# Kernel tuning notes

Measured on AMD Instinct MI355X. Metric: run time of the kernel, lower is better.

The kernel has to match this reference:

```python
import jax, jax.numpy as jnp
import numpy as np

B, N, D, M, C = 4, 256, 128, 128, 128


def _lin_init(key, din, dout):
    # torch nn.Linear default: U(-1/sqrt(din), 1/sqrt(din)) for weight and bias
    bound = 1.0 / np.sqrt(din)
    kw, kb = jax.random.split(key)
    W = jax.random.uniform(kw, (din, dout), jnp.float32, -bound, bound)
    b = jax.random.uniform(kb, (dout,), jnp.float32, -bound, bound)
    return W, b


def setup_inputs() -> dict:
    key = jax.random.key(0)
    k_h, k_adj, k1, k2, k3, k4 = jax.random.split(key, 6)
    h = jax.random.normal(k_h, (B, N, D), jnp.float32)
    adj = jax.random.uniform(k_adj, (B, N, N), jnp.float32)
    # msg MLP: Linear(2D -> M), SiLU, Linear(M -> M). Split first weight into
    # the h_i block (W1a) and h_j block (W1b) of the concatenated input.
    W1, b1 = _lin_init(k1, 2 * D, M)
    W1a, W1b = W1[:D], W1[D:]
    W2, b2 = _lin_init(k2, M, M)
    # to_c MLP: Linear(M -> M), SiLU, Linear(M -> C)
    Wc1, bc1 = _lin_init(k3, M, M)
    Wc2, bc2 = _lin_init(k4, M, C)
    return {"h": h, "adj": adj, "W1a": W1a, "W1b": W1b, "b1": b1,
            "W2": W2, "b2": b2, "Wc1": Wc1, "bc1": bc1, "Wc2": Wc2, "bc2": bc2}


def reference(h, adj, W1a, W1b, b1, W2, b2, Wc1, bc1, Wc2, bc2):
    n = h.shape[1]
    # First msg Linear on cat([h_i, h_j]) == h_i @ W1a + h_j @ W1b + b1.
    # Precompute per-node projections once instead of the (B,N,N,2D) pair tensor.
    pi = jnp.einsum('bnd,dm->bnm', h, W1a)           # (B,N,M) for destination i
    pj = jnp.einsum('bnd,dm->bnm', h, W1b)           # (B,N,M) for source j
    pre = pi[:, :, None, :] + pj[:, None, :, :] + b1  # (B,N,N,M)
    m = jnp.einsum('bijm,mk->bijk', jax.nn.silu(pre), W2) + b2  # (B,N,N,M)
    # zero self-messages (diagonal ignored), then weight by adjacency
    mask = (1.0 - jnp.eye(n, dtype=h.dtype))[None, :, :, None]
    m = m * mask * adj[..., None]
    # mean aggregation over source nodes j with clamped degree
    denom = jnp.clip(jnp.sum(adj, axis=-1, keepdims=True), 1.0)  # (B,N,1)
    m_agg = jnp.sum(m, axis=2) / denom                           # (B,N,M)
    c = jnp.einsum('bnm,mc->bnc', jax.nn.silu(jnp.einsum('bnm,mk->bnk', m_agg, Wc1) + bc1), Wc2) + bc2
    return c
```

## Files before the change

kernel.cpp:

```cpp
#include <hip/hip_runtime.h>
#include <math.h>

#define BB 4
#define NN 256
#define DD 128
#define MM 128
#define CC 128
#define ROWS (BB * NN)

static __device__ __forceinline__ float fast_exp2(float x) {
#if __has_builtin(__builtin_amdgcn_exp2f)
    return __builtin_amdgcn_exp2f(x);
#else
    return __exp2f(x);
#endif
}

static __device__ __forceinline__ float fast_rcp(float x) {
#if __has_builtin(__builtin_amdgcn_rcpf)
    return __builtin_amdgcn_rcpf(x);
#else
    return 1.0f / x;
#endif
}

static __device__ __forceinline__ float silu_f(float x) {
    float e = fast_exp2(-1.44269504088896340736f * x);
    return x * fast_rcp(1.0f + e);
}

template <int R>
__global__ __launch_bounds__(256) void k_proj(const float* __restrict__ h,
                                              const float* __restrict__ W1a,
                                              const float* __restrict__ W1b,
                                              const float* __restrict__ b1,
                                              float* __restrict__ pibias,
                                              float* __restrict__ pj) {
    __shared__ float sH[R * DD];
    __shared__ float sPA[R][MM];
    __shared__ float sPB[R][MM];
    const int t = threadIdx.x;
    const int m = t & 127;
    const int dh = t >> 7;
    const int row0 = blockIdx.x * R;

    const float* hbase = h + (size_t)row0 * DD;
    sH[t] = hbase[t];
    sH[t + 256] = hbase[t + 256];
    __syncthreads();

    const int d0 = dh * 64;
    float accA[R], accB[R];
    #pragma unroll
    for (int r = 0; r < R; ++r) { accA[r] = 0.0f; accB[r] = 0.0f; }

    #pragma unroll 8
    for (int d = d0; d < d0 + 64; ++d) {
        const float wa = W1a[d * MM + m];
        const float wb = W1b[d * MM + m];
        #pragma unroll
        for (int r = 0; r < R; ++r) {
            const float hv = sH[r * DD + d];
            accA[r] = fmaf(hv, wa, accA[r]);
            accB[r] = fmaf(hv, wb, accB[r]);
        }
    }

    if (dh == 1) {
        #pragma unroll
        for (int r = 0; r < R; ++r) { sPA[r][m] = accA[r]; sPB[r][m] = accB[r]; }
    }
    __syncthreads();
    if (dh == 0) {
        const float bias = b1[m];
        #pragma unroll
        for (int r = 0; r < R; ++r) {
            pibias[(row0 + r) * MM + m] = accA[r] + sPA[r][m] + bias;
            pj[(row0 + r) * MM + m]     = accB[r] + sPB[r][m];
        }
    }
}

__global__ __launch_bounds__(256) void k_msg(const float* __restrict__ adj,
                                             const float* __restrict__ pibias,
                                             const float* __restrict__ pj,
                                             float* __restrict__ S,
                                             float* __restrict__ beta) {
    __shared__ float sAdj[2][NN];
    __shared__ float sRed0[256];
    __shared__ float sRed1[256];
    __shared__ float sWred[2][4];

    const int t = threadIdx.x;
    const int pairIdx = blockIdx.x;
    const int b = pairIdx >> 7;
    const int i0 = (pairIdx & 127) * 2;
    const int row0 = b * NN + i0;

    const float* arow = adj + (size_t)row0 * NN;
    sAdj[0][t] = arow[t];
    sAdj[1][t] = arow[t + 256];
    __syncthreads();

    float v0 = sAdj[0][t];
    float v1 = sAdj[1][t];
    #pragma unroll
    for (int off = 32; off > 0; off >>= 1) {
        v0 += __shfl_xor(v0, off, 64);
        v1 += __shfl_xor(v1, off, 64);
    }
    if ((t & 63) == 0) { sWred[0][t >> 6] = v0; sWred[1][t >> 6] = v1; }
    __syncthreads();
    const float A0 = sWred[0][0] + sWred[0][1] + sWred[0][2] + sWred[0][3];
    const float A1 = sWred[1][0] + sWred[1][1] + sWred[1][2] + sWred[1][3];
    const float aii0 = sAdj[0][i0];
    const float aii1 = sAdj[1][i0 + 1];
    __syncthreads();
    if (t == 0) { sAdj[0][i0] = 0.0f; sAdj[1][i0 + 1] = 0.0f; }
    __syncthreads();

    const float inv0 = 1.0f / fmaxf(A0, 1.0f);
    const float inv1 = 1.0f / fmaxf(A1, 1.0f);

    const int m = t & 127;
    const int jh = t >> 7;
    const float pim0 = pibias[(size_t)row0 * MM + m];
    const float pim1 = pibias[(size_t)(row0 + 1) * MM + m];
    const float* __restrict__ pjB = pj + (size_t)b * NN * MM;

    float acc0 = 0.0f, acc1 = 0.0f;
    #pragma unroll 8
    for (int j = jh; j < NN; j += 2) {
        const float pjv = pjB[j * MM + m];
        const float w0 = sAdj[0][j];
        const float w1 = sAdj[1][j];
        acc0 = fmaf(w0, silu_f(pim0 + pjv), acc0);
        acc1 = fmaf(w1, silu_f(pim1 + pjv), acc1);
    }

    sRed0[t] = acc0;
    sRed1[t] = acc1;
    __syncthreads();
    if (t < 128) {
        S[(size_t)row0 * MM + t] = (sRed0[t] + sRed0[t + 128]) * inv0;
    } else {
        const int k = t - 128;
        S[(size_t)(row0 + 1) * MM + k] = (sRed1[k] + sRed1[k + 128]) * inv1;
    }
    if (t == 0) {
        beta[row0]     = (A0 - aii0) * inv0;
        beta[row0 + 1] = (A1 - aii1) * inv1;
    }
}

__device__ __forceinline__ void stage_dot4(const float* __restrict__ W,
                                           const float sCur[4][MM],
                                           int d0, int k, float acc[4]) {
    #pragma unroll
    for (int r = 0; r < 4; ++r) acc[r] = 0.0f;
    #pragma unroll 8
    for (int d = d0; d < d0 + 64; ++d) {
        const float wv = W[d * MM + k];
        #pragma unroll
        for (int r = 0; r < 4; ++r) acc[r] = fmaf(sCur[r][d], wv, acc[r]);
    }
}

template <int R>
__global__ __launch_bounds__(256) void k_out(const float* __restrict__ S,
                                             const float* __restrict__ beta,
                                             const float* __restrict__ W2,
                                             const float* __restrict__ b2,
                                             const float* __restrict__ Wc1,
                                             const float* __restrict__ bc1,
                                             const float* __restrict__ Wc2,
                                             const float* __restrict__ bc2,
                                             float* __restrict__ out) {
    __shared__ float sA[R][MM];
    __shared__ float sB[R][MM];
    __shared__ float sP[R][MM];
    const int t = threadIdx.x;
    const int k = t & 127;
    const int dh = t >> 7;
    const int d0 = dh * 64;
    const int row0 = blockIdx.x * R;

    float bet[R];
    #pragma unroll
    for (int r = 0; r < R; ++r) bet[r] = beta[row0 + r];

    {
        const float* sbase = S + (size_t)row0 * MM;
        ((float*)sA)[t]       = sbase[t];
        ((float*)sA)[t + 256] = sbase[t + 256];
    }
    __syncthreads();

    float acc[R];

    stage_dot4(W2, sA, d0, k, acc);
    if (dh == 1) {
        #pragma unroll
        for (int r = 0; r < R; ++r) sP[r][k] = acc[r];
    }
    __syncthreads();
    if (dh == 0) {
        const float b2k = b2[k];
        #pragma unroll
        for (int r = 0; r < R; ++r) sB[r][k] = acc[r] + sP[r][k] + bet[r] * b2k;
    }
    __syncthreads();

    stage_dot4(Wc1, sB, d0, k, acc);
    if (dh == 1) {
        #pragma unroll
        for (int r = 0; r < R; ++r) sP[r][k] = acc[r];
    }
    __syncthreads();
    if (dh == 0) {
        const float bc1k = bc1[k];
        #pragma unroll
        for (int r = 0; r < R; ++r) sA[r][k] = silu_f(acc[r] + sP[r][k] + bc1k);
    }
    __syncthreads();

    stage_dot4(Wc2, sA, d0, k, acc);
    if (dh == 1) {
        #pragma unroll
        for (int r = 0; r < R; ++r) sP[r][k] = acc[r];
    }
    __syncthreads();
    if (dh == 0) {
        const float bc2k = bc2[k];
        #pragma unroll
        for (int r = 0; r < R; ++r)
            out[(size_t)(row0 + r) * CC + k] = acc[r] + sP[r][k] + bc2k;
    }
}

extern "C" void kernel_launch(void* const* d_in, const int* in_sizes, int n_in,
                              void* d_out, int out_size, void* d_ws, size_t ws_size,
                              hipStream_t stream) {
    const float* h   = (const float*)d_in[0];
    const float* adj = (const float*)d_in[1];
    const float* W1a = (const float*)d_in[2];
    const float* W1b = (const float*)d_in[3];
    const float* b1  = (const float*)d_in[4];
    const float* W2  = (const float*)d_in[5];
    const float* b2  = (const float*)d_in[6];
    const float* Wc1 = (const float*)d_in[7];
    const float* bc1 = (const float*)d_in[8];
    const float* Wc2 = (const float*)d_in[9];
    const float* bc2 = (const float*)d_in[10];
    float* out = (float*)d_out;

    float* ws = (float*)d_ws;
    float* pibias = ws;
    float* pj     = ws + (size_t)ROWS * MM;
    float* S      = ws + (size_t)2 * ROWS * MM;
    float* beta   = ws + (size_t)3 * ROWS * MM;

    k_proj<4><<<ROWS / 4, 256, 0, stream>>>(h, W1a, W1b, b1, pibias, pj);
    k_msg<<<ROWS / 2, 256, 0, stream>>>(adj, pibias, pj, S, beta);
    k_out<4><<<ROWS / 4, 256, 0, stream>>>(S, beta, W2, b2, Wc1, bc1, Wc2, bc2, out);
}
```

Before: 104.8 us.

## Stage weights and pj tiles in LDS with float4 loads; split work by rows

All three kernels now copy weight or pj tiles into shared memory in chunks using float4 global loads, then compute from LDS instead of strided global reads. The projection and output kernels split threads by row pairs rather than by halves of the reduction dimension, which removes the shared-memory partial-sum combine step. The message kernel also hoists the adjacency and pibias loads ahead of the first barrier. The cost is more barriers per chunk and much larger LDS use per block, which may lower occupancy.

```diff
diff --git a/kernel.cpp b/kernel.cpp
--- a/kernel.cpp
+++ b/kernel.cpp
@@ -36,48 +36,56 @@
                                               const float* __restrict__ b1,
                                               float* __restrict__ pibias,
                                               float* __restrict__ pj) {
+    __shared__ float sWa[32 * MM];
+    __shared__ float sWb[32 * MM];
     __shared__ float sH[R * DD];
-    __shared__ float sPA[R][MM];
-    __shared__ float sPB[R][MM];
+
     const int t = threadIdx.x;
     const int m = t & 127;
-    const int dh = t >> 7;
+    const int rh = t >> 7;
     const int row0 = blockIdx.x * R;
+
+    const float bias = b1[m];
 
     const float* hbase = h + (size_t)row0 * DD;
     sH[t] = hbase[t];
     sH[t + 256] = hbase[t + 256];
-    __syncthreads();
-
-    const int d0 = dh * 64;
-    float accA[R], accB[R];
+
+    float accA[2] = {0.0f, 0.0f};
+    float accB[2] = {0.0f, 0.0f};
+
+    for (int c = 0; c < 4; ++c) {
+        __syncthreads();
+        const float4* ga = (const float4*)(W1a + (size_t)c * 32 * MM);
+        const float4* gb = (const float4*)(W1b + (size_t)c * 32 * MM);
+        float4* la = (float4*)sWa;
+        float4* lb = (float4*)sWb;
+        #pragma unroll
+        for (int i = 0; i < 4; ++i) {
+            la[t + 256 * i] = ga[t + 256 * i];
+            lb[t + 256 * i] = gb[t + 256 * i];
+        }
+        __syncthreads();
+
+        #pragma unroll 8
+        for (int dd = 0; dd < 32; ++dd) {
+            const int d = c * 32 + dd;
+            const float wa = sWa[dd * MM + m];
+            const float wb = sWb[dd * MM + m];
+            #pragma unroll
+            for (int r = 0; r < 2; ++r) {
+                const float hv = sH[(rh * 2 + r) * DD + d];
+                accA[r] = fmaf(hv, wa, accA[r]);
+                accB[r] = fmaf(hv, wb, accB[r]);
+            }
+        }
+    }
+
     #pragma unroll
-    for (int r = 0; r < R; ++r) { accA[r] = 0.0f; accB[r] = 0.0f; }
-
-    #pragma unroll 8
-    for (int d = d0; d < d0 + 64; ++d) {
-        const float wa = W1a[d * MM + m];
-        const float wb = W1b[d * MM + m];
-        #pragma unroll
-        for (int r = 0; r < R; ++r) {
-            const float hv = sH[r * DD + d];
-            accA[r] = fmaf(hv, wa, accA[r]);
-            accB[r] = fmaf(hv, wb, accB[r]);
-        }
-    }
-
-    if (dh == 1) {
-        #pragma unroll
-        for (int r = 0; r < R; ++r) { sPA[r][m] = accA[r]; sPB[r][m] = accB[r]; }
-    }
-    __syncthreads();
-    if (dh == 0) {
-        const float bias = b1[m];
-        #pragma unroll
-        for (int r = 0; r < R; ++r) {
-            pibias[(row0 + r) * MM + m] = accA[r] + sPA[r][m] + bias;
-            pj[(row0 + r) * MM + m]     = accB[r] + sPB[r][m];
-        }
+    for (int r = 0; r < 2; ++r) {
+        const int row = row0 + rh * 2 + r;
+        pibias[(size_t)row * MM + m] = accA[r] + bias;
+        pj[(size_t)row * MM + m]     = accB[r];
     }
 }
 
@@ -86,9 +94,9 @@
                                              const float* __restrict__ pj,
                                              float* __restrict__ S,
                                              float* __restrict__ beta) {
+    __shared__ float sPJ[64 * MM];
     __shared__ float sAdj[2][NN];
-    __shared__ float sRed0[256];
-    __shared__ float sRed1[256];
+    __shared__ float sRed[2][256];
     __shared__ float sWred[2][4];
 
     const int t = threadIdx.x;
@@ -97,13 +105,20 @@
     const int i0 = (pairIdx & 127) * 2;
     const int row0 = b * NN + i0;
 
+    const int m = t & 127;
+    const int jh = t >> 7;
+
     const float* arow = adj + (size_t)row0 * NN;
-    sAdj[0][t] = arow[t];
-    sAdj[1][t] = arow[t + 256];
-    __syncthreads();
-
-    float v0 = sAdj[0][t];
-    float v1 = sAdj[1][t];
+    const float a0v = arow[t];
+    const float a1v = arow[t + 256];
+    const float pim0 = pibias[(size_t)row0 * MM + m];
+    const float pim1 = pibias[(size_t)(row0 + 1) * MM + m];
+
+    sAdj[0][t] = a0v;
+    sAdj[1][t] = a1v;
+    __syncthreads();
+
+    float v0 = a0v, v1 = a1v;
     #pragma unroll
     for (int off = 32; off > 0; off >>= 1) {
         v0 += __shfl_xor(v0, off, 64);
@@ -117,35 +132,40 @@
     const float aii1 = sAdj[1][i0 + 1];
     __syncthreads();
     if (t == 0) { sAdj[0][i0] = 0.0f; sAdj[1][i0 + 1] = 0.0f; }
-    __syncthreads();
 
     const float inv0 = 1.0f / fmaxf(A0, 1.0f);
     const float inv1 = 1.0f / fmaxf(A1, 1.0f);
 
-    const int m = t & 127;
-    const int jh = t >> 7;
-    const float pim0 = pibias[(size_t)row0 * MM + m];
-    const float pim1 = pibias[(size_t)(row0 + 1) * MM + m];
     const float* __restrict__ pjB = pj + (size_t)b * NN * MM;
 
     float acc0 = 0.0f, acc1 = 0.0f;
-    #pragma unroll 8
-    for (int j = jh; j < NN; j += 2) {
-        const float pjv = pjB[j * MM + m];
-        const float w0 = sAdj[0][j];
-        const float w1 = sAdj[1][j];
-        acc0 = fmaf(w0, silu_f(pim0 + pjv), acc0);
-        acc1 = fmaf(w1, silu_f(pim1 + pjv), acc1);
-    }
-
-    sRed0[t] = acc0;
-    sRed1[t] = acc1;
+    for (int c = 0; c < 4; ++c) {
+        __syncthreads();
+        const float4* g = (const float4*)(pjB + (size_t)c * 64 * MM);
+        float4* l = (float4*)sPJ;
+        #pragma unroll
+        for (int i = 0; i < 8; ++i) l[t + 256 * i] = g[t + 256 * i];
+        __syncthreads();
+
+        #pragma unroll 8
+        for (int jj = jh; jj < 64; jj += 2) {
+            const int j = c * 64 + jj;
+            const float pjv = sPJ[jj * MM + m];
+            const float w0 = sAdj[0][j];
+            const float w1 = sAdj[1][j];
+            acc0 = fmaf(w0, silu_f(pim0 + pjv), acc0);
+            acc1 = fmaf(w1, silu_f(pim1 + pjv), acc1);
+        }
+    }
+
+    sRed[0][t] = acc0;
+    sRed[1][t] = acc1;
     __syncthreads();
     if (t < 128) {
-        S[(size_t)row0 * MM + t] = (sRed0[t] + sRed0[t + 128]) * inv0;
+        S[(size_t)row0 * MM + t] = (sRed[0][t] + sRed[0][t + 128]) * inv0;
     } else {
         const int k = t - 128;
-        S[(size_t)(row0 + 1) * MM + k] = (sRed1[k] + sRed1[k + 128]) * inv1;
+        S[(size_t)(row0 + 1) * MM + k] = (sRed[1][k] + sRed[1][k + 128]) * inv1;
     }
     if (t == 0) {
         beta[row0]     = (A0 - aii0) * inv0;
@@ -153,16 +173,25 @@
     }
 }
 
-__device__ __forceinline__ void stage_dot4(const float* __restrict__ W,
-                                           const float sCur[4][MM],
-                                           int d0, int k, float acc[4]) {
-    #pragma unroll
-    for (int r = 0; r < 4; ++r) acc[r] = 0.0f;
-    #pragma unroll 8
-    for (int d = d0; d < d0 + 64; ++d) {
-        const float wv = W[d * MM + k];
+__device__ __forceinline__ void matvec_staged(const float* __restrict__ W,
+                                              const float* __restrict__ src,
+                                              float* __restrict__ sW,
+                                              float acc[2], int t, int k, int rh) {
+    for (int c = 0; c < 2; ++c) {
+        __syncthreads();
+        const float4* g = (const float4*)(W + (size_t)c * 64 * MM);
+        float4* l = (float4*)sW;
         #pragma unroll
-        for (int r = 0; r < 4; ++r) acc[r] = fmaf(sCur[r][d], wv, acc[r]);
+        for (int i = 0; i < 8; ++i) l[t + 256 * i] = g[t + 256 * i];
+        __syncthreads();
+
+        #pragma unroll 8
+        for (int dd = 0; dd < 64; ++dd) {
+            const int d = c * 64 + dd;
+            const float wv = sW[dd * MM + k];
+            acc[0] = fmaf(src[(rh * 2 + 0) * MM + d], wv, acc[0]);
+            acc[1] = fmaf(src[(rh * 2 + 1) * MM + d], wv, acc[1]);
+        }
     }
 }
 
@@ -176,66 +205,44 @@
                                              const float* __restrict__ Wc2,
                                              const float* __restrict__ bc2,
                                              float* __restrict__ out) {
-    __shared__ float sA[R][MM];
-    __shared__ float sB[R][MM];
-    __shared__ float sP[R][MM];
+    __shared__ float sW[64 * MM];
+    __shared__ float sA[R * MM];
+    __shared__ float sB[R * MM];
+
     const int t = threadIdx.x;
     const int k = t & 127;
-    const int dh = t >> 7;
-    const int d0 = dh * 64;
+    const int rh = t >> 7;
     const int row0 = blockIdx.x * R;
 
-    float bet[R];
-    #pragma unroll
-    for (int r = 0; r < R; ++r) bet[r] = beta[row0 + r];
-
-    {
-        const float* sbase = S + (size_t)row0 * MM;
-        ((float*)sA)[t]       = sbase[t];
-        ((float*)sA)[t + 256] = sbase[t + 256];
-    }
-    __syncthreads();
-
-    float acc[R];
-
-    stage_dot4(W2, sA, d0, k, acc);
-    if (dh == 1) {
-        #pragma unroll
-        for (int r = 0; r < R; ++r) sP[r][k] = acc[r];
-    }
-    __syncthreads();
-    if (dh == 0) {
-        const float b2k = b2[k];
-        #pragma unroll
-        for (int r = 0; r < R; ++r) sB[r][k] = acc[r] + sP[r][k] + bet[r] * b2k;
-    }
-    __syncthreads();
-
-    stage_dot4(Wc1, sB, d0, k, acc);
-    if (dh == 1) {
-        #pragma unroll
-        for (int r = 0; r < R; ++r) sP[r][k] = acc[r];
-    }
-    __syncthreads();
-    if (dh == 0) {
-        const float bc1k = bc1[k];
-        #pragma unroll
-        for (int r = 0; r < R; ++r) sA[r][k] = silu_f(acc[r] + sP[r][k] + bc1k);
-    }
-    __syncthreads();
-
-    stage_dot4(Wc2, sA, d0, k, acc);
-    if (dh == 1) {
-        #pragma unroll
-        for (int r = 0; r < R; ++r) sP[r][k] = acc[r];
-    }
-    __syncthreads();
-    if (dh == 0) {
-        const float bc2k = bc2[k];
-        #pragma unroll
-        for (int r = 0; r < R; ++r)
-            out[(size_t)(row0 + r) * CC + k] = acc[r] + sP[r][k] + bc2k;
-    }
+    const float bet0 = beta[row0 + rh * 2];
+    const float bet1 = beta[row0 + rh * 2 + 1];
+    const float b2k  = b2[k];
+    const float bc1k = bc1[k];
+    const float bc2k = bc2[k];
+
+    const float* sbase = S + (size_t)row0 * MM;
+    sA[t] = sbase[t];
+    sA[t + 256] = sbase[t + 256];
+
+    float acc[2];
+
+    acc[0] = bet0 * b2k;
+    acc[1] = bet1 * b2k;
+    matvec_staged(W2, sA, sW, acc, t, k, rh);
+    sB[(rh * 2 + 0) * MM + k] = acc[0];
+    sB[(rh * 2 + 1) * MM + k] = acc[1];
+
+    acc[0] = bc1k;
+    acc[1] = bc1k;
+    matvec_staged(Wc1, sB, sW, acc, t, k, rh);
+    sA[(rh * 2 + 0) * MM + k] = silu_f(acc[0]);
+    sA[(rh * 2 + 1) * MM + k] = silu_f(acc[1]);
+
+    acc[0] = bc2k;
+    acc[1] = bc2k;
+    matvec_staged(Wc2, sA, sW, acc, t, k, rh);
+    out[(size_t)(row0 + rh * 2 + 0) * CC + k] = acc[0];
+    out[(size_t)(row0 + rh * 2 + 1) * CC + k] = acc[1];
 }
 
 extern "C" void kernel_launch(void* const* d_in, const int* in_sizes, int n_in,
```

New measurement: 105.8 us. No clear change (+0.9%).
